# Optimization experiments

Measured on AMD Instinct MI355X. Metric: run time of the kernel, lower is better.

Reference implementation:

```python
import jax, jax.numpy as jnp
import numpy as np

SIGMA = 1.0
NUM_CLASSES = 10


def setup_inputs() -> dict:
    key = jax.random.key(0)
    k1, k2, k3, k4 = jax.random.split(key, 4)
    ns, nt, d = 4096, 4096, 256
    return {
        "source_feature": jax.random.normal(k1, (ns, d), dtype=jnp.float32),
        "source_label": jax.random.randint(k2, (ns,), 0, NUM_CLASSES),
        "target_feature": jax.random.normal(k3, (nt, d), dtype=jnp.float32),
        "class_weight": jax.random.uniform(k4, (NUM_CLASSES,), dtype=jnp.float32),
    }


def _rbf_gram(x, y, sigma):
    # K[i, j] = exp(-||x_i - y_j||^2 / (2*sigma)); [n, m]
    x2 = jnp.sum(x * x, axis=-1)  # [n]
    y2 = jnp.sum(y * y, axis=-1)  # [m]
    sq = x2[:, None] + y2[None, :] - 2.0 * (x @ y.T)
    sq = jnp.maximum(sq, 0.0)
    return jnp.exp(-sq / (2.0 * sigma))


def reference(source_feature, source_label, target_feature, class_weight):
    ns = source_feature.shape[0]
    nt = target_feature.shape[0]
    w = class_weight[source_label]          # [ns] per-sample weight
    n = jnp.sum(w)                          # weighted source count

    Kss = _rbf_gram(source_feature, source_feature, SIGMA)  # [ns, ns]
    Ktt = _rbf_gram(target_feature, target_feature, SIGMA)  # [nt, nt]
    Kst = _rbf_gram(source_feature, target_feature, SIGMA)  # [ns, nt]

    first = jnp.einsum('i,ij,j->', w, Kss, w)
    sec = jnp.sum(Ktt)
    third = jnp.einsum('i,ij->', w, Kst)

    return first / (n * n) + sec / (nt * nt) - 2.0 * third / (n * nt)
```

## Files before the change

### kernel.cpp

```cpp
#include <hip/hip_runtime.h>
#include <hip/hip_bf16.h>


typedef short bf16x8 __attribute__((ext_vector_type(8)));
typedef float f32x4 __attribute__((ext_vector_type(4)));

#define D 256

static __device__ __forceinline__ unsigned short f32_to_bf16(float f) {
    unsigned int x = __float_as_uint(f);
    unsigned int r = (x + 0x7FFFu + ((x >> 16) & 1u)) >> 16;
    return (unsigned short)r;
}


__global__ __launch_bounds__(256) void prep_kernel(
    const float* __restrict__ sf, const float* __restrict__ tf,
    const int* __restrict__ lbl, const float* __restrict__ cw,
    unsigned short* __restrict__ sfb, unsigned short* __restrict__ tfb,
    float* __restrict__ x2s, float* __restrict__ x2t,
    float* __restrict__ wv, int ns)
{
    int row = blockIdx.x * 4 + (threadIdx.x >> 6);
    int t = threadIdx.x & 63;
    bool is_src = row < ns;
    int r = is_src ? row : row - ns;
    const float* src = (is_src ? sf : tf) + (size_t)r * D;
    unsigned short* dstb = is_src ? sfb : tfb;

    float4 v = ((const float4*)src)[t];
    ushort4 u;
    u.x = f32_to_bf16(v.x); u.y = f32_to_bf16(v.y);
    u.z = f32_to_bf16(v.z); u.w = f32_to_bf16(v.w);

    int g = r >> 4, rr = r & 15;
    int k = t * 4;
    int s_ = k >> 5, kr = (k >> 3) & 3, off = k & 7;
    size_t idx = ((size_t)((g * 8 + s_) * 64) + kr * 16 + rr) * 8 + off;
    *(ushort4*)(dstb + idx) = u;

    float s = v.x * v.x + v.y * v.y + v.z * v.z + v.w * v.w;
    #pragma unroll
    for (int o = 32; o; o >>= 1) s += __shfl_xor(s, o);

    if (t == 0) {
        if (is_src) { wv[r] = cw[lbl[r]]; x2s[r] = s; }
        else        { x2t[r] = s; }
    }
}

__global__ __launch_bounds__(256, 3) void gram_kernel(
    const unsigned short* __restrict__ sfb, const unsigned short* __restrict__ tfb,
    const float* __restrict__ x2s, const float* __restrict__ x2t,
    const float* __restrict__ wv, float* __restrict__ bout,
    int ti_s, int ti_t)
{
    int tri_s = ti_s * (ti_s + 1) / 2;
    int tri_t = ti_t * (ti_t + 1) / 2;
    int blk = blockIdx.x;

    int mode, bi, bj;
    const unsigned short *X, *Y;
    const float *x2xp, *x2yp;
    if (blk < tri_s + tri_t) {
        int T, idx;
        if (blk < tri_s) { mode = 0; idx = blk; T = ti_s; X = sfb; Y = sfb; x2xp = x2s; x2yp = x2s; }
        else { mode = 1; idx = blk - tri_s; T = ti_t; X = tfb; Y = tfb; x2xp = x2t; x2yp = x2t; }
        bi = (int)((2.0f * T + 1.0f -
                    sqrtf((float)((2 * T + 1) * (2 * T + 1) - 8 * idx))) * 0.5f);
        if (bi < 0) bi = 0;
        if (bi > T - 1) bi = T - 1;
        int base = bi * (2 * T - bi + 1) / 2;
        while (base > idx) { --bi; base = bi * (2 * T - bi + 1) / 2; }
        while (idx >= base + (T - bi)) { base += (T - bi); ++bi; }
        bj = bi + (idx - base);
    } else {
        int idx = blk - tri_s - tri_t;
        mode = 2; bi = idx / ti_t; bj = idx % ti_t;
        X = sfb; Y = tfb; x2xp = x2s; x2yp = x2t;
    }
    float factor = (mode != 2 && bi != bj) ? 2.0f : 1.0f;

    int wid = threadIdx.x >> 6;
    int lane = threadIdx.x & 63;
    int wr = wid >> 1, wc = wid & 1;
    int R0 = bi * 128 + wr * 64;
    int C0 = bj * 128 + wc * 64;

    const unsigned short* XA = X + (size_t)(R0 >> 4) * 4096 + lane * 8;
    const unsigned short* YB = Y + (size_t)(C0 >> 4) * 4096 + lane * 8;

    f32x4 acc[4][4] = {};
    bf16x8 af[2][4], bfr[2][4];
    #pragma unroll
    for (int m = 0; m < 4; ++m) {
        af[0][m]  = *(const bf16x8*)(XA + m * 8 * 512);
        bfr[0][m] = *(const bf16x8*)(YB + m * 8 * 512);
    }
    #pragma unroll
    for (int s = 0; s < 8; ++s) {
        const int cur = s & 1, nxt = cur ^ 1;
        if (s < 7) {
            #pragma unroll
            for (int m = 0; m < 4; ++m) {
                af[nxt][m]  = *(const bf16x8*)(XA + (m * 8 + s + 1) * 512);
                bfr[nxt][m] = *(const bf16x8*)(YB + (m * 8 + s + 1) * 512);
            }
        }
        #pragma unroll
        for (int m = 0; m < 4; ++m)
            #pragma unroll
            for (int n = 0; n < 4; ++n)
                acc[m][n] = __builtin_amdgcn_mfma_f32_16x16x32_bf16(
                    af[cur][m], bfr[cur][n], acc[m][n], 0, 0, 0);
    }

    int crow = (lane >> 4) * 4;
    int ccol = lane & 15;
    float s = 0.0f;
    #pragma unroll
    for (int m = 0; m < 4; ++m) {
        #pragma unroll
        for (int r = 0; r < 4; ++r) {
            int gr = R0 + 16 * m + crow + r;
            float rx2 = x2xp[gr];
            float rw = (mode != 1) ? wv[gr] : 1.0f;
            #pragma unroll
            for (int n = 0; n < 4; ++n) {
                int gc = C0 + 16 * n + ccol;
                float S = acc[m][n][r];
                float sq = fmaxf(x2yp[gc] + rx2 - 2.0f * S, 0.0f);
                float K = __expf(-0.5f * sq);
                if (mode != 2 && gr == gc) K = 1.0f;
                float wf = (mode == 0) ? rw * wv[gc] : rw;
                s += wf * K;
            }
        }
    }
    s *= factor;
    #pragma unroll
    for (int o = 32; o; o >>= 1) s += __shfl_xor(s, o);

    __shared__ float bsum[4];
    if (lane == 0) bsum[wid] = s;
    __syncthreads();
    if (threadIdx.x == 0)
        bout[blk] = (bsum[0] + bsum[1]) + (bsum[2] + bsum[3]);
}

__global__ __launch_bounds__(1024) void reduce_kernel(
    const float* __restrict__ wv, int ns,
    const float* __restrict__ bout, int tri_s, int tri_t, int nb,
    float* __restrict__ out, int nt)
{
    int tid = threadIdx.x;
    float n = 0.0f, a0 = 0.0f, a1 = 0.0f, a2 = 0.0f;
    for (int i = tid; i < ns; i += 1024) n += wv[i];
    for (int i = tid; i < nb; i += 1024) {
        float v = bout[i];
        if (i < tri_s) a0 += v;
        else if (i < tri_s + tri_t) a1 += v;
        else a2 += v;
    }
    #pragma unroll
    for (int o = 32; o; o >>= 1) {
        n  += __shfl_xor(n, o);
        a0 += __shfl_xor(a0, o);
        a1 += __shfl_xor(a1, o);
        a2 += __shfl_xor(a2, o);
    }
    __shared__ float ln[16], l0[16], l1[16], l2[16];
    int w = tid >> 6;
    if ((tid & 63) == 0) { ln[w] = n; l0[w] = a0; l1[w] = a1; l2[w] = a2; }
    __syncthreads();
    if (tid == 0) {
        float N = 0, A0 = 0, A1 = 0, A2 = 0;
        #pragma unroll
        for (int i = 0; i < 16; ++i) { N += ln[i]; A0 += l0[i]; A1 += l1[i]; A2 += l2[i]; }
        float fnt = (float)nt;
        out[0] = A0 / (N * N) + A1 / (fnt * fnt) - 2.0f * A2 / (N * fnt);
    }
}

extern "C" void kernel_launch(void* const* d_in, const int* in_sizes, int n_in,
                              void* d_out, int out_size, void* d_ws, size_t ws_size,
                              hipStream_t stream) {
    const float* sf = (const float*)d_in[0];
    const int* lbl = (const int*)d_in[1];
    const float* tf = (const float*)d_in[2];
    const float* cw = (const float*)d_in[3];
    float* out = (float*)d_out;

    int ns = in_sizes[1];
    int d = in_sizes[0] / ns;
    int nt = in_sizes[2] / d;

    char* p = (char*)d_ws;
    unsigned short* sfb = (unsigned short*)p;  p += (size_t)ns * d * sizeof(unsigned short);
    unsigned short* tfb = (unsigned short*)p;  p += (size_t)nt * d * sizeof(unsigned short);
    float* x2s = (float*)p;                    p += (size_t)ns * sizeof(float);
    float* x2t = (float*)p;                    p += (size_t)nt * sizeof(float);
    float* wv  = (float*)p;                    p += (size_t)ns * sizeof(float);
    float* bout = (float*)p;

    prep_kernel<<<(ns + nt) / 4, 256, 0, stream>>>(sf, tf, lbl, cw, sfb, tfb,
                                                   x2s, x2t, wv, ns);

    int ti_s = ns / 128, ti_t = nt / 128;
    int tri_s = ti_s * (ti_s + 1) / 2;
    int tri_t = ti_t * (ti_t + 1) / 2;
    int nblocks = tri_s + tri_t + ti_s * ti_t;
    gram_kernel<<<nblocks, 256, 0, stream>>>(sfb, tfb, x2s, x2t, wv, bout,
                                             ti_s, ti_t);

    reduce_kernel<<<1, 1024, 0, stream>>>(wv, ns, bout, tri_s, tri_t, nblocks,
                                          out, nt);
}
```

Before: 50.33 us.

## Stage gram tiles through LDS with async global_load_lds double buffering

Replaces per-wave direct global loads of A/B fragments with block-cooperative staging into shared memory via global_load_lds, double-buffered across four K chunks. Each 128x128 block now loads its A and B panels once and shares them among four waves, instead of each wave loading its own 64-row slices, which halves global/L2 traffic. The cost is 64KB of LDS per block, lower occupancy (launch bounds reduced from 3 to 2 blocks per CU), and extra barriers per chunk.

```diff
diff --git a/kernel.cpp b/kernel.cpp
--- a/kernel.cpp
+++ b/kernel.cpp
@@ -49,7 +49,14 @@
     }
 }
 
-__global__ __launch_bounds__(256, 3) void gram_kernel(
+static __device__ __forceinline__ void gload_lds16(const unsigned short* g,
+                                                   unsigned short* l) {
+    __builtin_amdgcn_global_load_lds(
+        (const __attribute__((address_space(1))) void*)g,
+        (__attribute__((address_space(3))) void*)l, 16, 0, 0);
+}
+
+__global__ __launch_bounds__(256, 2) void gram_kernel(
     const unsigned short* __restrict__ sfb, const unsigned short* __restrict__ tfb,
     const float* __restrict__ x2s, const float* __restrict__ x2t,
     const float* __restrict__ wv, float* __restrict__ bout,
@@ -81,40 +88,57 @@
     }
     float factor = (mode != 2 && bi != bj) ? 2.0f : 1.0f;
 
+    __shared__ unsigned short lds[2][32][512];
+
     int wid = threadIdx.x >> 6;
     int lane = threadIdx.x & 63;
     int wr = wid >> 1, wc = wid & 1;
+
+    const unsigned short* Abase = X + (size_t)(bi * 8) * 4096;
+    const unsigned short* Bbase = Y + (size_t)(bj * 8) * 4096;
+
+    auto STAGE = [&](int c, int buf) {
+        #pragma unroll
+        for (int j = 0; j < 8; ++j) {
+            int u = wid * 8 + j;
+            int isB = u >> 4;
+            int g = (u & 15) >> 1;
+            int sl = u & 1;
+            const unsigned short* src =
+                (isB ? Bbase : Abase) + ((size_t)g * 8 + c * 2 + sl) * 512 + lane * 8;
+            gload_lds16(src, &lds[buf][u][0]);
+        }
+    };
+
+    f32x4 acc[4][4] = {};
+
+    STAGE(0, 0);
+    __syncthreads();
+    #pragma unroll
+    for (int c = 0; c < 4; ++c) {
+        if (c < 3) STAGE(c + 1, (c + 1) & 1);
+        const int buf = c & 1;
+        #pragma unroll
+        for (int sl = 0; sl < 2; ++sl) {
+            bf16x8 a[4], b[4];
+            #pragma unroll
+            for (int m = 0; m < 4; ++m)
+                a[m] = *(const bf16x8*)&lds[buf][(wr * 4 + m) * 2 + sl][lane * 8];
+            #pragma unroll
+            for (int n = 0; n < 4; ++n)
+                b[n] = *(const bf16x8*)&lds[buf][16 + (wc * 4 + n) * 2 + sl][lane * 8];
+            #pragma unroll
+            for (int m = 0; m < 4; ++m)
+                #pragma unroll
+                for (int n = 0; n < 4; ++n)
+                    acc[m][n] = __builtin_amdgcn_mfma_f32_16x16x32_bf16(
+                        a[m], b[n], acc[m][n], 0, 0, 0);
+        }
+        __syncthreads();
+    }
+
     int R0 = bi * 128 + wr * 64;
     int C0 = bj * 128 + wc * 64;
-
-    const unsigned short* XA = X + (size_t)(R0 >> 4) * 4096 + lane * 8;
-    const unsigned short* YB = Y + (size_t)(C0 >> 4) * 4096 + lane * 8;
-
-    f32x4 acc[4][4] = {};
-    bf16x8 af[2][4], bfr[2][4];
-    #pragma unroll
-    for (int m = 0; m < 4; ++m) {
-        af[0][m]  = *(const bf16x8*)(XA + m * 8 * 512);
-        bfr[0][m] = *(const bf16x8*)(YB + m * 8 * 512);
-    }
-    #pragma unroll
-    for (int s = 0; s < 8; ++s) {
-        const int cur = s & 1, nxt = cur ^ 1;
-        if (s < 7) {
-            #pragma unroll
-            for (int m = 0; m < 4; ++m) {
-                af[nxt][m]  = *(const bf16x8*)(XA + (m * 8 + s + 1) * 512);
-                bfr[nxt][m] = *(const bf16x8*)(YB + (m * 8 + s + 1) * 512);
-            }
-        }
-        #pragma unroll
-        for (int m = 0; m < 4; ++m)
-            #pragma unroll
-            for (int n = 0; n < 4; ++n)
-                acc[m][n] = __builtin_amdgcn_mfma_f32_16x16x32_bf16(
-                    af[cur][m], bfr[cur][n], acc[m][n], 0, 0, 0);
-    }
-
     int crow = (lane >> 4) * 4;
     int ccol = lane & 15;
     float s = 0.0f;
```

Measured after the change: 53.58 us. +6.5%, slower.
